# Kernel tuning notes

Hardware: AMD Instinct MI355X
Metric: run time of the kernel (lower is better)

The kernel has to match this reference:

```python
import jax, jax.numpy as jnp
import numpy as np

POOLED_H, POOLED_W = 7, 7
SPATIAL_SCALE = 0.25
SAMPLING_RATIO = 2
N, C, H, W = 2, 256, 200, 200
K = 1000
IMG = 800.0  # image-space extent (H/spatial_scale)


def setup_inputs() -> dict:
    key = jax.random.key(0)
    k1, k2, k3 = jax.random.split(key, 3)
    inp = jax.random.normal(k1, (N, C, H, W), dtype=jnp.float32)
    # boxes in image coordinates (x1,y1,x2,y2) with x1<=x2, y1<=y2
    pts = jax.random.uniform(k2, (K, 2, 2), dtype=jnp.float32) * (IMG - 1.0)  # [K,2,(x,y)]
    lo = jnp.min(pts, axis=1)  # [K,2] -> x1,y1
    hi = jnp.max(pts, axis=1)  # [K,2] -> x2,y2
    b = jax.random.randint(k3, (K,), 0, N).astype(jnp.float32)
    rois = jnp.concatenate([b[:, None], lo[:, :1], lo[:, 1:], hi[:, :1], hi[:, 1:]], axis=1)
    return {"input": inp, "rois": rois}


def _interp_axis(coord, size):
    """Per-axis bilinear setup (torchvision roi_align semantics).
    coord: [...], returns (low_idx, high_idx, low_w, high_w, valid)."""
    valid = (coord >= -1.0) & (coord <= size)
    c = jnp.clip(coord, 0.0, None)
    low = jnp.floor(c).astype(jnp.int32)
    over = low >= size - 1
    low = jnp.where(over, size - 1, low)
    high = jnp.where(over, size - 1, low + 1)
    frac = jnp.where(over, 0.0, c - low.astype(c.dtype))  # l (weight for high)
    return low, high, 1.0 - frac, frac, valid


def roi_align_fwd(input, rois):
    Nn, Cc, Hh, Ww = input.shape
    sr = SAMPLING_RATIO
    b = rois[:, 0].astype(jnp.int32)                       # [K]
    x1, y1, x2, y2 = [rois[:, i] * SPATIAL_SCALE for i in (1, 2, 3, 4)]
    roi_w = jnp.maximum(x2 - x1, 1.0)
    roi_h = jnp.maximum(y2 - y1, 1.0)
    bin_h = roi_h / POOLED_H
    bin_w = roi_w / POOLED_W

    ph = jnp.arange(POOLED_H, dtype=jnp.float32)
    pw = jnp.arange(POOLED_W, dtype=jnp.float32)
    off = (jnp.arange(sr, dtype=jnp.float32) + 0.5) / sr
    # sample coordinates: [K, PH*sr] and [K, PW*sr]
    ys = (y1[:, None, None] + (ph[None, :, None] + off[None, None, :]) * bin_h[:, None, None]).reshape(rois.shape[0], POOLED_H * sr)
    xs = (x1[:, None, None] + (pw[None, :, None] + off[None, None, :]) * bin_w[:, None, None]).reshape(rois.shape[0], POOLED_W * sr)

    yl, yh, wyl, wyh, vy = _interp_axis(ys, Hh)
    xl, xh, wxl, wxh, vx = _interp_axis(xs, Ww)

    bi = b[:, None, None]

    def gather(yi, xi):  # -> [K, Gy, Gx, C]
        return input[bi, :, yi[:, :, None], xi[:, None, :]]

    val = (
        (wyl[:, :, None] * wxl[:, None, :])[..., None] * gather(yl, xl)
        + (wyl[:, :, None] * wxh[:, None, :])[..., None] * gather(yl, xh)
        + (wyh[:, :, None] * wxl[:, None, :])[..., None] * gather(yh, xl)
        + (wyh[:, :, None] * wxh[:, None, :])[..., None] * gather(yh, xh)
    )  # [K, Gy, Gx, C]
    mask = (vy[:, :, None] & vx[:, None, :]).astype(val.dtype)[..., None]
    val = val * mask
    Kk = rois.shape[0]
    out = val.reshape(Kk, POOLED_H, sr, POOLED_W, sr, Cc).sum(axis=(2, 4)) / (sr * sr)
    return jnp.transpose(out, (0, 3, 1, 2))  # [K, C, PH, PW]


def reference(input, rois):
    return roi_align_fwd(input, rois)
```

## Files before the change

kernel.cpp:

```cpp
#include <hip/hip_runtime.h>
#include <hip/hip_bf16.h>

constexpr int Nn = 2, Cc = 256, Hh = 200, Ww = 200, Kk = 1000;
constexpr int PH = 7, PW = 7, SR = 2;
constexpr float SCALE = 0.25f;
constexpr int HWsz = Hh * Ww;

__global__ __launch_bounds__(256) void transpose_to_nhwc_bf16(
    const float* __restrict__ in, __hip_bfloat16* __restrict__ out) {
  __shared__ float tile[64][65];
  const int hw0 = blockIdx.x * 64;
  const int c0  = blockIdx.y * 64;
  const int b   = blockIdx.z;
  const int lane = threadIdx.x & 63;
  const int row  = threadIdx.x >> 6;

#pragma unroll
  for (int i = 0; i < 16; ++i) {
    const int cc = row + i * 4;
    tile[cc][lane] = in[(size_t)(b * Cc + c0 + cc) * HWsz + hw0 + lane];
  }
  __syncthreads();
#pragma unroll
  for (int i = 0; i < 16; ++i) {
    const int hh = row + i * 4;
    out[((size_t)b * HWsz + hw0 + hh) * Cc + c0 + lane] =
        __float2bfloat16(tile[lane][hh]);
  }
}

__device__ __forceinline__ int sidx(int c, int p) {
  return c * 49 + p + 13 * (c >> 2);
}

__global__ __launch_bounds__(448, 7) void roi_align_nhwc_bf16(
    const ushort* __restrict__ feat, const float* __restrict__ rois,
    float* __restrict__ out) {
  __shared__ float stage[6704];

  const int k    = blockIdx.x;
  const int half = blockIdx.y;
  const int ph   = (int)(threadIdx.x >> 6);
  const int lane = (int)(threadIdx.x & 63);
  const int ixl  = lane >> 5;
  const int cq   = lane & 31;

  const float* r = rois + k * 5;
  const int b = (int)r[0];
  const float x1 = r[1] * SCALE;
  const float y1 = r[2] * SCALE;
  const float x2 = r[3] * SCALE;
  const float y2 = r[4] * SCALE;
  const float bin_w = fmaxf(x2 - x1, 1.0f) * (1.0f / PW);
  const float bin_h = fmaxf(y2 - y1, 1.0f) * (1.0f / PH);

  const ushort4* fb =
      (const ushort4*)(feat + (size_t)b * HWsz * Cc) + half * 32 + cq;

  float4 acc[PW];
#pragma unroll
  for (int i = 0; i < PW; ++i) acc[i] = make_float4(0.f, 0.f, 0.f, 0.f);

  auto bf2f = [](ushort u) -> float {
    return __uint_as_float((unsigned)u << 16);
  };

  const float x_off = ((float)ixl + 0.5f) * 0.5f;

#pragma unroll
  for (int iy = 0; iy < SR; ++iy) {
    const float y  = y1 + ((float)ph + ((float)iy + 0.5f) * 0.5f) * bin_h;
    const bool vy  = (y >= -1.0f) && (y <= (float)Hh);
    const float cy = fmaxf(y, 0.0f);
    int yl = (int)cy;
    int yh;
    float fy;
    if (yl >= Hh - 1) { yl = Hh - 1; yh = Hh - 1; fy = 0.0f; }
    else              { yh = yl + 1; fy = cy - (float)yl; }
    float wyl = 1.0f - fy, wyh = fy;
    if (!vy) { wyl = 0.0f; wyh = 0.0f; }
    const int ylb = yl * Ww, yhb = yh * Ww;

#pragma unroll
    for (int pw = 0; pw < PW; ++pw) {
      const float x  = x1 + ((float)pw + x_off) * bin_w;
      const bool vx  = (x >= -1.0f) && (x <= (float)Ww);
      const float cx = fmaxf(x, 0.0f);
      int xl = (int)cx;
      int xh;
      float fx;
      if (xl >= Ww - 1) { xl = Ww - 1; xh = Ww - 1; fx = 0.0f; }
      else              { xh = xl + 1; fx = cx - (float)xl; }
      float wxl = 1.0f - fx, wxh = fx;
      if (!vx) { wxl = 0.0f; wxh = 0.0f; }

      const float w00 = wyl * wxl, w01 = wyl * wxh;
      const float w10 = wyh * wxl, w11 = wyh * wxh;

      const ushort4 v00 = fb[(ylb + xl) * 64];
      const ushort4 v01 = fb[(ylb + xh) * 64];
      const ushort4 v10 = fb[(yhb + xl) * 64];
      const ushort4 v11 = fb[(yhb + xh) * 64];

      acc[pw].x = fmaf(w00, bf2f(v00.x), fmaf(w01, bf2f(v01.x),
                  fmaf(w10, bf2f(v10.x), fmaf(w11, bf2f(v11.x), acc[pw].x))));
      acc[pw].y = fmaf(w00, bf2f(v00.y), fmaf(w01, bf2f(v01.y),
                  fmaf(w10, bf2f(v10.y), fmaf(w11, bf2f(v11.y), acc[pw].y))));
      acc[pw].z = fmaf(w00, bf2f(v00.z), fmaf(w01, bf2f(v01.z),
                  fmaf(w10, bf2f(v10.z), fmaf(w11, bf2f(v11.z), acc[pw].z))));
      acc[pw].w = fmaf(w00, bf2f(v00.w), fmaf(w01, bf2f(v01.w),
                  fmaf(w10, bf2f(v10.w), fmaf(w11, bf2f(v11.w), acc[pw].w))));
    }
  }

#pragma unroll
  for (int pw = 0; pw < PW; ++pw) {
    acc[pw].x += __shfl_xor(acc[pw].x, 32);
    acc[pw].y += __shfl_xor(acc[pw].y, 32);
    acc[pw].z += __shfl_xor(acc[pw].z, 32);
    acc[pw].w += __shfl_xor(acc[pw].w, 32);
  }

  const float inv = 1.0f / (SR * SR);
  if (lane < 32) {
    const int c0 = cq * 4;
    const int p = ph * PW;
#pragma unroll
    for (int pw = 0; pw < PW; ++pw) {
      stage[sidx(c0 + 0, p + pw)] = acc[pw].x * inv;
      stage[sidx(c0 + 1, p + pw)] = acc[pw].y * inv;
      stage[sidx(c0 + 2, p + pw)] = acc[pw].z * inv;
      stage[sidx(c0 + 3, p + pw)] = acc[pw].w * inv;
    }
  }
  __syncthreads();

  const size_t obase = (size_t)k * (Cc * PH * PW) + (size_t)half * (128 * PH * PW);
#pragma unroll
  for (int i = 0; i < 14; ++i) {
    const int idx = i * 448 + (int)threadIdx.x;
    const int c = idx / 49, p = idx - c * 49;
    out[obase + idx] = stage[sidx(c, p)];
  }
}

extern "C" void kernel_launch(void* const* d_in, const int* in_sizes, int n_in,
                              void* d_out, int out_size, void* d_ws, size_t ws_size,
                              hipStream_t stream) {
  const float* inp  = (const float*)d_in[0];
  const float* rois = (const float*)d_in[1];
  float* out = (float*)d_out;

  __hip_bfloat16* nhwc = (__hip_bfloat16*)d_ws;
  transpose_to_nhwc_bf16<<<dim3(HWsz / 64, Cc / 64, Nn), 256, 0, stream>>>(inp, nhwc);
  roi_align_nhwc_bf16<<<dim3(Kk, 2), 448, 0, stream>>>((const ushort*)nhwc, rois, out);
}
```

Before: 72.40 us.

## Sort ROIs by batch and y-center and process them with a persistent work-stealing kernel

Adds a single-block counting-sort kernel that orders ROIs by batch index and vertical centre. The ROI-align kernel becomes persistent: 1024 blocks pull (roi, channel-half) units from a global atomic counter in sorted order, so blocks running at the same time tend to touch nearby feature rows. Output stores become nontemporal and occupancy hints are lowered. In exchange it adds a serial one-block sort launch, a memset and atomic dispatch overhead per unit, which may cost more than the cache locality saves.

```diff
diff --git a/kernel.cpp b/kernel.cpp
--- a/kernel.cpp
+++ b/kernel.cpp
@@ -5,6 +5,7 @@
 constexpr int PH = 7, PW = 7, SR = 2;
 constexpr float SCALE = 0.25f;
 constexpr int HWsz = Hh * Ww;
+constexpr unsigned NUNITS = 2 * Kk;
 
 __global__ __launch_bounds__(256) void transpose_to_nhwc_bf16(
     const float* __restrict__ in, __hip_bfloat16* __restrict__ out) {
@@ -29,118 +30,157 @@
   }
 }
 
+__global__ __launch_bounds__(1024) void sort_rois(
+    const float* __restrict__ rois, unsigned* __restrict__ order) {
+  __shared__ unsigned hist[400];
+  __shared__ unsigned base[400];
+  const int tid = (int)threadIdx.x;
+  if (tid < 400) hist[tid] = 0;
+  __syncthreads();
+  for (int k = tid; k < Kk; k += 1024) {
+    const float* r = rois + k * 5;
+    int yc = (int)(0.5f * (r[2] + r[4]) * SCALE);
+    yc = yc < 0 ? 0 : (yc > 199 ? 199 : yc);
+    atomicAdd(&hist[(int)r[0] * 200 + yc], 1u);
+  }
+  __syncthreads();
+  if (tid == 0) {
+    unsigned s = 0;
+    for (int i = 0; i < 400; ++i) { base[i] = s; s += hist[i]; }
+  }
+  __syncthreads();
+  for (int k = tid; k < Kk; k += 1024) {
+    const float* r = rois + k * 5;
+    int yc = (int)(0.5f * (r[2] + r[4]) * SCALE);
+    yc = yc < 0 ? 0 : (yc > 199 ? 199 : yc);
+    const unsigned pos = atomicAdd(&base[(int)r[0] * 200 + yc], 1u);
+    order[pos] = (unsigned)k;
+  }
+}
+
 __device__ __forceinline__ int sidx(int c, int p) {
   return c * 49 + p + 13 * (c >> 2);
 }
 
-__global__ __launch_bounds__(448, 7) void roi_align_nhwc_bf16(
+__global__ __launch_bounds__(448, 4) void roi_align_ws(
     const ushort* __restrict__ feat, const float* __restrict__ rois,
-    float* __restrict__ out) {
+    const unsigned* __restrict__ order, float* __restrict__ out,
+    unsigned* __restrict__ counter) {
   __shared__ float stage[6704];
-
-  const int k    = blockIdx.x;
-  const int half = blockIdx.y;
-  const int ph   = (int)(threadIdx.x >> 6);
-  const int lane = (int)(threadIdx.x & 63);
+  __shared__ unsigned s_unit;
+
+  const int tid  = (int)threadIdx.x;
+  const int ph   = tid >> 6;
+  const int lane = tid & 63;
   const int ixl  = lane >> 5;
   const int cq   = lane & 31;
-
-  const float* r = rois + k * 5;
-  const int b = (int)r[0];
-  const float x1 = r[1] * SCALE;
-  const float y1 = r[2] * SCALE;
-  const float x2 = r[3] * SCALE;
-  const float y2 = r[4] * SCALE;
-  const float bin_w = fmaxf(x2 - x1, 1.0f) * (1.0f / PW);
-  const float bin_h = fmaxf(y2 - y1, 1.0f) * (1.0f / PH);
-
-  const ushort4* fb =
-      (const ushort4*)(feat + (size_t)b * HWsz * Cc) + half * 32 + cq;
-
-  float4 acc[PW];
-#pragma unroll
-  for (int i = 0; i < PW; ++i) acc[i] = make_float4(0.f, 0.f, 0.f, 0.f);
 
   auto bf2f = [](ushort u) -> float {
     return __uint_as_float((unsigned)u << 16);
   };
-
   const float x_off = ((float)ixl + 0.5f) * 0.5f;
 
-#pragma unroll
-  for (int iy = 0; iy < SR; ++iy) {
-    const float y  = y1 + ((float)ph + ((float)iy + 0.5f) * 0.5f) * bin_h;
-    const bool vy  = (y >= -1.0f) && (y <= (float)Hh);
-    const float cy = fmaxf(y, 0.0f);
-    int yl = (int)cy;
-    int yh;
-    float fy;
-    if (yl >= Hh - 1) { yl = Hh - 1; yh = Hh - 1; fy = 0.0f; }
-    else              { yh = yl + 1; fy = cy - (float)yl; }
-    float wyl = 1.0f - fy, wyh = fy;
-    if (!vy) { wyl = 0.0f; wyh = 0.0f; }
-    const int ylb = yl * Ww, yhb = yh * Ww;
+  for (;;) {
+    if (tid == 0) s_unit = atomicAdd(counter, 1u);
+    __syncthreads();
+    const unsigned unit = s_unit;
+    if (unit >= NUNITS) return;
+
+    const int k    = (int)order[unit >> 1];
+    const int half = (int)(unit & 1);
+
+    const float* r = rois + k * 5;
+    const int b = (int)r[0];
+    const float x1 = r[1] * SCALE;
+    const float y1 = r[2] * SCALE;
+    const float x2 = r[3] * SCALE;
+    const float y2 = r[4] * SCALE;
+    const float bin_w = fmaxf(x2 - x1, 1.0f) * (1.0f / PW);
+    const float bin_h = fmaxf(y2 - y1, 1.0f) * (1.0f / PH);
+
+    const ushort4* fb =
+        (const ushort4*)(feat + (size_t)b * HWsz * Cc) + half * 32 + cq;
+
+    float4 acc[PW];
+#pragma unroll
+    for (int i = 0; i < PW; ++i) acc[i] = make_float4(0.f, 0.f, 0.f, 0.f);
+
+#pragma unroll
+    for (int iy = 0; iy < SR; ++iy) {
+      const float y  = y1 + ((float)ph + ((float)iy + 0.5f) * 0.5f) * bin_h;
+      const bool vy  = (y >= -1.0f) && (y <= (float)Hh);
+      const float cy = fmaxf(y, 0.0f);
+      int yl = (int)cy;
+      int yh;
+      float fy;
+      if (yl >= Hh - 1) { yl = Hh - 1; yh = Hh - 1; fy = 0.0f; }
+      else              { yh = yl + 1; fy = cy - (float)yl; }
+      float wyl = 1.0f - fy, wyh = fy;
+      if (!vy) { wyl = 0.0f; wyh = 0.0f; }
+      const int ylb = yl * Ww, yhb = yh * Ww;
+
+#pragma unroll
+      for (int pw = 0; pw < PW; ++pw) {
+        const float x  = x1 + ((float)pw + x_off) * bin_w;
+        const bool vx  = (x >= -1.0f) && (x <= (float)Ww);
+        const float cx = fmaxf(x, 0.0f);
+        int xl = (int)cx;
+        int xh;
+        float fx;
+        if (xl >= Ww - 1) { xl = Ww - 1; xh = Ww - 1; fx = 0.0f; }
+        else              { xh = xl + 1; fx = cx - (float)xl; }
+        float wxl = 1.0f - fx, wxh = fx;
+        if (!vx) { wxl = 0.0f; wxh = 0.0f; }
+
+        const float w00 = wyl * wxl, w01 = wyl * wxh;
+        const float w10 = wyh * wxl, w11 = wyh * wxh;
+
+        const ushort4 v00 = fb[(ylb + xl) * 64];
+        const ushort4 v01 = fb[(ylb + xh) * 64];
+        const ushort4 v10 = fb[(yhb + xl) * 64];
+        const ushort4 v11 = fb[(yhb + xh) * 64];
+
+        acc[pw].x = fmaf(w00, bf2f(v00.x), fmaf(w01, bf2f(v01.x),
+                    fmaf(w10, bf2f(v10.x), fmaf(w11, bf2f(v11.x), acc[pw].x))));
+        acc[pw].y = fmaf(w00, bf2f(v00.y), fmaf(w01, bf2f(v01.y),
+                    fmaf(w10, bf2f(v10.y), fmaf(w11, bf2f(v11.y), acc[pw].y))));
+        acc[pw].z = fmaf(w00, bf2f(v00.z), fmaf(w01, bf2f(v01.z),
+                    fmaf(w10, bf2f(v10.z), fmaf(w11, bf2f(v11.z), acc[pw].z))));
+        acc[pw].w = fmaf(w00, bf2f(v00.w), fmaf(w01, bf2f(v01.w),
+                    fmaf(w10, bf2f(v10.w), fmaf(w11, bf2f(v11.w), acc[pw].w))));
+      }
+    }
 
 #pragma unroll
     for (int pw = 0; pw < PW; ++pw) {
-      const float x  = x1 + ((float)pw + x_off) * bin_w;
-      const bool vx  = (x >= -1.0f) && (x <= (float)Ww);
-      const float cx = fmaxf(x, 0.0f);
-      int xl = (int)cx;
-      int xh;
-      float fx;
-      if (xl >= Ww - 1) { xl = Ww - 1; xh = Ww - 1; fx = 0.0f; }
-      else              { xh = xl + 1; fx = cx - (float)xl; }
-      float wxl = 1.0f - fx, wxh = fx;
-      if (!vx) { wxl = 0.0f; wxh = 0.0f; }
-
-      const float w00 = wyl * wxl, w01 = wyl * wxh;
-      const float w10 = wyh * wxl, w11 = wyh * wxh;
-
-      const ushort4 v00 = fb[(ylb + xl) * 64];
-      const ushort4 v01 = fb[(ylb + xh) * 64];
-      const ushort4 v10 = fb[(yhb + xl) * 64];
-      const ushort4 v11 = fb[(yhb + xh) * 64];
-
-      acc[pw].x = fmaf(w00, bf2f(v00.x), fmaf(w01, bf2f(v01.x),
-                  fmaf(w10, bf2f(v10.x), fmaf(w11, bf2f(v11.x), acc[pw].x))));
-      acc[pw].y = fmaf(w00, bf2f(v00.y), fmaf(w01, bf2f(v01.y),
-                  fmaf(w10, bf2f(v10.y), fmaf(w11, bf2f(v11.y), acc[pw].y))));
-      acc[pw].z = fmaf(w00, bf2f(v00.z), fmaf(w01, bf2f(v01.z),
-                  fmaf(w10, bf2f(v10.z), fmaf(w11, bf2f(v11.z), acc[pw].z))));
-      acc[pw].w = fmaf(w00, bf2f(v00.w), fmaf(w01, bf2f(v01.w),
-                  fmaf(w10, bf2f(v10.w), fmaf(w11, bf2f(v11.w), acc[pw].w))));
-    }
-  }
-
-#pragma unroll
-  for (int pw = 0; pw < PW; ++pw) {
-    acc[pw].x += __shfl_xor(acc[pw].x, 32);
-    acc[pw].y += __shfl_xor(acc[pw].y, 32);
-    acc[pw].z += __shfl_xor(acc[pw].z, 32);
-    acc[pw].w += __shfl_xor(acc[pw].w, 32);
-  }
-
-  const float inv = 1.0f / (SR * SR);
-  if (lane < 32) {
-    const int c0 = cq * 4;
-    const int p = ph * PW;
-#pragma unroll
-    for (int pw = 0; pw < PW; ++pw) {
-      stage[sidx(c0 + 0, p + pw)] = acc[pw].x * inv;
-      stage[sidx(c0 + 1, p + pw)] = acc[pw].y * inv;
-      stage[sidx(c0 + 2, p + pw)] = acc[pw].z * inv;
-      stage[sidx(c0 + 3, p + pw)] = acc[pw].w * inv;
-    }
-  }
-  __syncthreads();
-
-  const size_t obase = (size_t)k * (Cc * PH * PW) + (size_t)half * (128 * PH * PW);
-#pragma unroll
-  for (int i = 0; i < 14; ++i) {
-    const int idx = i * 448 + (int)threadIdx.x;
-    const int c = idx / 49, p = idx - c * 49;
-    out[obase + idx] = stage[sidx(c, p)];
+      acc[pw].x += __shfl_xor(acc[pw].x, 32);
+      acc[pw].y += __shfl_xor(acc[pw].y, 32);
+      acc[pw].z += __shfl_xor(acc[pw].z, 32);
+      acc[pw].w += __shfl_xor(acc[pw].w, 32);
+    }
+
+    const float inv = 1.0f / (SR * SR);
+    if (lane < 32) {
+      const int c0 = cq * 4;
+      const int p = ph * PW;
+#pragma unroll
+      for (int pw = 0; pw < PW; ++pw) {
+        stage[sidx(c0 + 0, p + pw)] = acc[pw].x * inv;
+        stage[sidx(c0 + 1, p + pw)] = acc[pw].y * inv;
+        stage[sidx(c0 + 2, p + pw)] = acc[pw].z * inv;
+        stage[sidx(c0 + 3, p + pw)] = acc[pw].w * inv;
+      }
+    }
+    __syncthreads();
+
+    const size_t obase =
+        (size_t)k * (Cc * PH * PW) + (size_t)half * (128 * PH * PW);
+#pragma unroll
+    for (int i = 0; i < 14; ++i) {
+      const int idx = i * 448 + tid;
+      const int c = idx / 49, p = idx - c * 49;
+      __builtin_nontemporal_store(stage[sidx(c, p)], &out[obase + idx]);
+    }
   }
 }
 
@@ -152,6 +192,11 @@
   float* out = (float*)d_out;
 
   __hip_bfloat16* nhwc = (__hip_bfloat16*)d_ws;
+  unsigned* counter = (unsigned*)((char*)d_ws + (48u << 20));
+  unsigned* order   = counter + 64;
+
   transpose_to_nhwc_bf16<<<dim3(HWsz / 64, Cc / 64, Nn), 256, 0, stream>>>(inp, nhwc);
-  roi_align_nhwc_bf16<<<dim3(Kk, 2), 448, 0, stream>>>((const ushort*)nhwc, rois, out);
-}
+  sort_rois<<<dim3(1), 1024, 0, stream>>>(rois, order);
+  hipMemsetAsync(counter, 0, sizeof(unsigned), stream);
+  roi_align_ws<<<dim3(1024), 448, 0, stream>>>((const ushort*)nhwc, rois, order, out, counter);
+}
```

After: 82.94 us. 1.15x slower.
